# Kernel tuning notes

Hardware: AMD Instinct MI355X
Metric: run time of the kernel (lower is better)

## Reference

```python
import jax, jax.numpy as jnp
import numpy as np

NS, NG, NV = 16, 8, 8          # scalar, gate, vector(l=1) multiplicities
CIN = 8                        # input irreps: 8x0
COUT1 = NS + NG + 3 * NV       # 48 channels into gate
CMID = NS + 3 * NV             # 40 channels after gate
KS = 3                         # kernel size
NB = 4                         # radial basis count
P = KS ** 3
BN_EPS = 1e-5

EPS3 = (jnp.zeros((3, 3, 3))
        .at[0, 1, 2].set(1.).at[1, 2, 0].set(1.).at[2, 0, 1].set(1.)
        .at[0, 2, 1].set(-1.).at[2, 1, 0].set(-1.).at[1, 0, 2].set(-1.))


def _lattice():
    c = jnp.linspace(-1., 1., KS)
    g = jnp.stack(jnp.meshgrid(c, c, c, indexing='ij'), -1).reshape(-1, 3)  # [P,3]
    r = jnp.linalg.norm(g, axis=-1)
    rhat = jnp.where(r[:, None] > 0., g / jnp.maximum(r, 1e-9)[:, None], 0.)
    sh0 = jnp.ones_like(r)             # Y_0, component normalization
    sh1 = jnp.sqrt(3.) * rhat          # Y_1, component normalization
    # soft_one_hot_linspace(r, 0, 1, NB, 'smooth_finite', cutoff=False)
    centers = jnp.linspace(0., 1., NB)
    step = centers[1] - centers[0]
    d = (r[:, None] - centers[None, :]) / step
    emb = jnp.where(jnp.abs(d) < 1.,
                    1.14136 * jnp.exp(2.) * jnp.exp(-1. / jnp.maximum(1. - d ** 2, 1e-9)),
                    0.)
    return sh0, sh1, emb


def _kernel1(w1, emb, sh0, sh1):
    # per-lattice-point tensor-product weights: 8x0 (x) (0+1) -> 16x0 + 8x0 + 8x1
    W = (emb @ w1) / KS ** 1.5                 # [P, 256]
    w_ss = W[:, :128].reshape(P, CIN, NS)
    w_sg = W[:, 128:192].reshape(P, CIN, NG)
    w_sv = W[:, 192:256].reshape(P, CIN, NV)
    a = 1. / jnp.sqrt(8.)                      # fan-in per output irrep
    Km = jnp.zeros((P, CIN, COUT1))
    Km = Km.at[:, :, :NS].set(a * w_ss * sh0[:, None, None])
    Km = Km.at[:, :, NS:NS + NG].set(a * w_sg * sh0[:, None, None])
    kv = a * jnp.einsum('pij,pm->pijm', w_sv, sh1)
    return Km.at[:, :, NS + NG:].set(kv.reshape(P, CIN, 3 * NV))


def _kernel2(w2, emb, sh0, sh1):
    # (16x0 + 8x1) (x) (0+1) -> 16x0 + 8x0 + 8x1 with l<=1 CG paths
    W = (emb @ w2) / KS ** 1.5                 # [P, 832]
    w_ss = W[:, 0:256].reshape(P, NS, NS)
    w_sg = W[:, 256:384].reshape(P, NS, NG)
    w_sv = W[:, 384:512].reshape(P, NS, NV)
    w_vv0 = W[:, 512:576].reshape(P, NV, NV)
    w_vs = W[:, 576:704].reshape(P, NV, NS)
    w_vg = W[:, 704:768].reshape(P, NV, NG)
    w_vv1 = W[:, 768:832].reshape(P, NV, NV)
    a_s = 1. / jnp.sqrt(16. + 8.)
    a_v = 1. / jnp.sqrt(16. + 8. + 8.)
    Km = jnp.zeros((P, CMID, COUT1))
    Km = Km.at[:, :NS, :NS].set(a_s * w_ss * sh0[:, None, None])
    Km = Km.at[:, :NS, NS:NS + NG].set(a_s * w_sg * sh0[:, None, None])
    Km = Km.at[:, :NS, NS + NG:].set(
        (a_v * jnp.einsum('pij,pm->pijm', w_sv, sh1)).reshape(P, NS, 3 * NV))
    ks = (a_s / jnp.sqrt(3.)) * jnp.einsum('puj,pm->pumj', w_vs, sh1)
    kg = (a_s / jnp.sqrt(3.)) * jnp.einsum('puj,pm->pumj', w_vg, sh1)
    kv0 = a_v * jnp.einsum('puj,p,mn->pumjn', w_vv0, sh0, jnp.eye(3))
    kv1 = (a_v / jnp.sqrt(6.)) * jnp.einsum('puj,msn,ps->pumjn', w_vv1, EPS3, sh1)
    Km = Km.at[:, NS:, :NS].set(ks.reshape(P, 3 * NV, NS))
    Km = Km.at[:, NS:, NS:NS + NG].set(kg.reshape(P, 3 * NV, NG))
    return Km.at[:, NS:, NS + NG:].set((kv0 + kv1).reshape(P, 3 * NV, 3 * NV))


def _conv3d(x, Km, cin):
    ker = Km.reshape(KS, KS, KS, cin, COUT1).transpose(4, 3, 0, 1, 2)  # [O,I,k,k,k]
    return jax.lax.conv_general_dilated(
        x, ker, (1, 1, 1), 'SAME',
        dimension_numbers=('NCDHW', 'OIDHW', 'NCDHW'))


def _batchnorm(x, ws, bs, wv):
    # e3nn BatchNorm, training statistics, reduce='mean'; x channel-last [...,48]
    s = x[..., :NS + NG]
    mu = s.mean(axis=(0, 1, 2, 3))
    s = s - mu
    var = (s ** 2).mean(axis=(0, 1, 2, 3))
    s = s / jnp.sqrt(var + BN_EPS) * ws + bs
    v = x[..., NS + NG:].reshape(x.shape[:-1] + (NV, 3))
    n2 = (v ** 2).sum(-1).mean(axis=(0, 1, 2, 3))   # [NV]
    v = v * (((n2 + BN_EPS) ** -0.5) * wv)[:, None]
    return jnp.concatenate([s, v.reshape(x.shape[:-1] + (3 * NV,))], -1)


def _gate(x):
    # Gate: relu on scalars, sigmoid gates multiply l=1 fields
    s = jax.nn.relu(x[..., :NS])
    g = jax.nn.sigmoid(x[..., NS:NS + NG])
    v = x[..., NS + NG:].reshape(x.shape[:-1] + (NV, 3)) * g[..., None]
    return jnp.concatenate([s, v.reshape(x.shape[:-1] + (3 * NV,))], -1)


def _forward(x, w1, sc1, w2, sc2_s, sc2_v,
             bn1_ws, bn1_bs, bn1_wv, bn2_ws, bn2_bs, bn2_wv):
    sh0, sh1, emb = _lattice()
    y = _conv3d(x, _kernel1(w1, emb, sh0, sh1), CIN)
    y = y.at[:, :NS + NG].add(
        jnp.einsum('bixyz,io->boxyz', x, sc1) / jnp.sqrt(8.))  # self-connection
    y = jnp.moveaxis(y, 1, -1)
    y = _gate(_batchnorm(y, bn1_ws, bn1_bs, bn1_wv))           # dropout p=0: identity
    y = jnp.moveaxis(y, -1, 1)                                 # [B, 40, X, Y, Z]
    z = _conv3d(y, _kernel2(w2, emb, sh0, sh1), CMID)
    z = z.at[:, :NS + NG].add(
        jnp.einsum('bixyz,io->boxyz', y[:, :NS], sc2_s) / jnp.sqrt(16.))
    yv = y[:, NS:].reshape(y.shape[0], NV, 3, *y.shape[2:])
    scv = jnp.einsum('bumxyz,uj->bjmxyz', yv, sc2_v) / jnp.sqrt(8.)
    z = z.at[:, NS + NG:].add(scv.reshape(z.shape[0], 3 * NV, *z.shape[2:]))
    z = jnp.moveaxis(z, 1, -1)
    z = _gate(_batchnorm(z, bn2_ws, bn2_bs, bn2_wv))
    return jnp.moveaxis(z, -1, 1)                              # [B, 40, X, Y, Z]


def setup_inputs() -> dict:
    key = jax.random.key(0)
    ks = jax.random.split(key, 8)
    B, S = 1, 64
    return {
        'x': jax.random.normal(ks[0], (B, CIN, S, S, S), jnp.float32),
        'w1': jax.random.normal(ks[1], (NB, 256), jnp.float32),
        'sc1': jax.random.normal(ks[2], (CIN, NS + NG), jnp.float32),
        'w2': jax.random.normal(ks[3], (NB, 832), jnp.float32),
        'sc2_s': jax.random.normal(ks[4], (NS, NS + NG), jnp.float32),
        'sc2_v': jax.random.normal(ks[5], (NV, NV), jnp.float32),
        'bn1_ws': jnp.ones((NS + NG,), jnp.float32),
        'bn1_bs': jnp.zeros((NS + NG,), jnp.float32),
        'bn1_wv': jnp.ones((NV,), jnp.float32),
        'bn2_ws': jnp.ones((NS + NG,), jnp.float32),
        'bn2_bs': jnp.zeros((NS + NG,), jnp.float32),
        'bn2_wv': jnp.ones((NV,), jnp.float32),
    }


def reference(x, w1, sc1, w2, sc2_s, sc2_v,
              bn1_ws, bn1_bs, bn1_wv, bn2_ws, bn2_bs, bn2_wv):
    return _forward(x, w1, sc1, w2, sc2_s, sc2_v,
                    bn1_ws, bn1_bs, bn1_wv, bn2_ws, bn2_bs, bn2_wv)
```

## Files before the change

kernel.cpp:

```cpp
#include <hip/hip_runtime.h>
#include <math.h>

#define N3 262144


#define TBL_TOTAL 1728

__device__ inline void lattice_emb(int p, float* embr) {
    int i = p / 9, j = (p / 3) % 3, k = p % 3;
    float gx = (float)(i - 1), gy = (float)(j - 1), gz = (float)(k - 1);
    float r = sqrtf(gx * gx + gy * gy + gz * gz);
    const float centers[4] = {0.f, 0.33333334f, 0.6666667f, 1.f};
    const float step = 0.33333334f;
    #pragma unroll
    for (int b = 0; b < 4; b++) {
        float dd = (r - centers[b]) / step;
        float e = 0.f;
        if (fabsf(dd) < 1.f)
            e = 1.14136f * expf(2.f) * expf(-1.f / fmaxf(1.f - dd * dd, 1e-9f));
        embr[b] = e;
    }
}

__global__ __launch_bounds__(256) void build_tables_kernel(
        const float* __restrict__ w1,  const float* __restrict__ sc1,
        const float* __restrict__ w2,  const float* __restrict__ sc2s,
        const float* __restrict__ sc2v, float* __restrict__ T) {
    int gid = blockIdx.x * 256 + threadIdx.x;
    if (gid >= TBL_TOTAL) return;

    const float inv_ks15 = 0.19245008972987526f;
    const float s3   = 1.7320508075688772f;
    const float a1   = 0.35355339059327373f;
    const float a_s  = 0.2041241452319315f;
    const float a_v  = 0.17677669529663687f;
    const float a_s3 = 0.11785113019775793f;
    const float a_v6 = 0.07216878364870322f;

    float embC[4], embF[4];
    lattice_emb(13, embC);
    lattice_emb(22, embF);

    auto WC1 = [&](int c) { float s=0.f;
        #pragma unroll
        for (int b=0;b<4;b++) s += embC[b]*w1[b*256+c]; return s*inv_ks15; };
    auto WF1 = [&](int c) { float s=0.f;
        #pragma unroll
        for (int b=0;b<4;b++) s += embF[b]*w1[b*256+c]; return s*inv_ks15; };
    auto WC2 = [&](int c) { float s=0.f;
        #pragma unroll
        for (int b=0;b<4;b++) s += embC[b]*w2[b*832+c]; return s*inv_ks15; };
    auto WF2 = [&](int c) { float s=0.f;
        #pragma unroll
        for (int b=0;b<4;b++) s += embF[b]*w2[b*832+c]; return s*inv_ks15; };

    float val = 0.f;
    if (gid < 192) {
        int i = gid / 24, o = gid % 24;
        int c = (o < 16) ? i * 16 + o : 128 + i * 8 + (o - 16);
        val = a1 * WC1(c) + a1 * sc1[i * 24 + o];
    } else if (gid < 384) {
        int r = gid - 192; int i = r / 24, o = r % 24;
        int c = (o < 16) ? i * 16 + o : 128 + i * 8 + (o - 16);
        val = a1 * WF1(c);
    } else if (gid < 448) {
        int r = gid - 384; int i = r / 8, jj = r % 8;
        val = a1 * s3 * WF1(192 + i * 8 + jj);
    } else if (gid < 832) {
        int r = gid - 448; int i = r / 24, o = r % 24;
        int c = (o < 16) ? i * 16 + o : 256 + i * 8 + (o - 16);
        val = a_s * WC2(c) + 0.25f * sc2s[i * 24 + o];
    } else if (gid < 1216) {
        int r = gid - 832; int i = r / 24, o = r % 24;
        int c = (o < 16) ? i * 16 + o : 256 + i * 8 + (o - 16);
        val = a_s * WF2(c);
    } else if (gid < 1344) {
        int r = gid - 1216; int i = r / 8, jj = r % 8;
        val = a_v * s3 * WF2(384 + i * 8 + jj);
    } else if (gid < 1536) {
        int r = gid - 1344; int u = r / 24, o = r % 24;
        int c = (o < 16) ? 576 + u * 16 + o : 704 + u * 8 + (o - 16);
        val = a_s3 * s3 * WF2(c);
    } else if (gid < 1600) {
        int r = gid - 1536; int u = r / 8, jj = r % 8;
        val = a_v * WC2(512 + u * 8 + jj) + a1 * sc2v[u * 8 + jj];
    } else if (gid < 1664) {
        int r = gid - 1600; int u = r / 8, jj = r % 8;
        val = a_v * WF2(512 + u * 8 + jj);
    } else {
        int r = gid - 1664; int u = r / 8, jj = r % 8;
        val = a_v6 * s3 * WF2(768 + u * 8 + jj);
    }
    T[gid] = val;
}

__device__ inline float4 f4z() { return make_float4(0.f, 0.f, 0.f, 0.f); }
__device__ inline float4 f4add(float4 a, float4 b) {
    return make_float4(a.x+b.x, a.y+b.y, a.z+b.z, a.w+b.w); }
__device__ inline float4 f4sub(float4 a, float4 b) {
    return make_float4(a.x-b.x, a.y-b.y, a.z-b.z, a.w-b.w); }
__device__ inline float4 f4fma(float s, float4 a, float4 c) {
    return make_float4(fmaf(s,a.x,c.x), fmaf(s,a.y,c.y), fmaf(s,a.z,c.z), fmaf(s,a.w,c.w)); }
__device__ inline float f4sum(float4 a) { return a.x+a.y+a.z+a.w; }
__device__ inline float f4dot(float4 a) { return a.x*a.x+a.y*a.y+a.z*a.z+a.w*a.w; }

#define LQ5(BP, C_, DM_, DP_, HM_, HP_)                                       \
    {                                                                         \
        const float* _p = (BP);                                               \
        C_  = *(const float4*)_p;                                             \
        DM_ = dmok ? *(const float4*)(_p - 4096) : f4z();                     \
        DP_ = dpok ? *(const float4*)(_p + 4096) : f4z();                     \
        HM_ = hmok ? *(const float4*)(_p -   64) : f4z();                     \
        HP_ = hpok ? *(const float4*)(_p +   64) : f4z();                     \
    }

#define WQ(C_, WM_, WP_)                                                      \
    {                                                                         \
        float _lw = __shfl_up((C_).w, 1, 64);                                 \
        float _rw = __shfl_down((C_).x, 1, 64);                               \
        WM_ = make_float4(wL ? 0.f : _lw, (C_).x, (C_).y, (C_).z);            \
        WP_ = make_float4((C_).y, (C_).z, (C_).w, wR ? 0.f : _rw);            \
    }

__global__ __launch_bounds__(128) void conv1_kernel(const float* __restrict__ x,
                                                    const float* __restrict__ Tg,
                                                    float* __restrict__ out,
                                                    float* __restrict__ stats) {
    __shared__ float T[448];
    __shared__ float red[2][48];
    for (int t = threadIdx.x; t < 448; t += 128) T[t] = Tg[t];
    __syncthreads();

    const int ohalf = blockIdx.y;
    int idx = blockIdx.x * 512 + threadIdx.x * 4;
    int w0 = idx & 63, h = (idx >> 6) & 63, d = idx >> 12;
    bool dmok = d > 0, dpok = d < 63, hmok = h > 0, hpok = h < 63;
    bool wL = (w0 == 0), wR = (w0 == 60);

    float4 acc[24];
    #pragma unroll
    for (int o = 0; o < 24; o++) acc[o] = f4z();

    if (ohalf == 0) {
        float4 nc, ndm, ndp, nhm, nhp;
        LQ5(x + idx, nc, ndm, ndp, nhm, nhp);
        #pragma unroll 1
        for (int i = 0; i < 8; i++) {
            float4 c = nc, dmq = ndm, dpq = ndp, hmq = nhm, hpq = nhp;
            if (i < 7) LQ5(x + (i + 1) * N3 + idx, nc, ndm, ndp, nhm, nhp);
            float4 wmq, wpq; WQ(c, wmq, wpq);
            float4 S = f4add(f4add(f4add(dmq, dpq), f4add(hmq, hpq)), f4add(wmq, wpq));
            const float* tc = &T[i * 24];
            const float* tf = &T[192 + i * 24];
            #pragma unroll
            for (int o = 0; o < 24; o++)
                acc[o] = f4fma(tc[o], c, f4fma(tf[o], S, acc[o]));
        }
    } else {
        float4 nc, ndm, ndp, nhm, nhp;
        LQ5(x + idx, nc, ndm, ndp, nhm, nhp);
        #pragma unroll 1
        for (int i = 0; i < 8; i++) {
            float4 c = nc, dmq = ndm, dpq = ndp, hmq = nhm, hpq = nhp;
            if (i < 7) LQ5(x + (i + 1) * N3 + idx, nc, ndm, ndp, nhm, nhp);
            float4 wmq, wpq; WQ(c, wmq, wpq);
            float4 Dd = f4sub(dpq, dmq), Dh = f4sub(hpq, hmq), Dw = f4sub(wpq, wmq);
            const float* tv = &T[384 + i * 8];
            #pragma unroll
            for (int jj = 0; jj < 8; jj++) {
                float wv = tv[jj];
                acc[jj * 3 + 0] = f4fma(wv, Dd, acc[jj * 3 + 0]);
                acc[jj * 3 + 1] = f4fma(wv, Dh, acc[jj * 3 + 1]);
                acc[jj * 3 + 2] = f4fma(wv, Dw, acc[jj * 3 + 2]);
            }
        }
    }

    int obase = ohalf * 24;
    #pragma unroll
    for (int o = 0; o < 24; o++)
        *(float4*)(out + (obase + o) * N3 + idx) = acc[o];

    int lane = threadIdx.x & 63, wvx = threadIdx.x >> 6;
    if (ohalf == 0) {
        #pragma unroll
        for (int q = 0; q < 48; q++) {
            float val = (q < 24) ? f4sum(acc[q]) : f4dot(acc[q - 24]);
            #pragma unroll
            for (int mq = 32; mq >= 1; mq >>= 1) val += __shfl_xor(val, mq, 64);
            if (lane == 0) red[wvx][q] = val;
        }
        __syncthreads();
        if (threadIdx.x < 48)
            atomicAdd(&stats[threadIdx.x], red[0][threadIdx.x] + red[1][threadIdx.x]);
    } else {
        #pragma unroll
        for (int q = 0; q < 24; q++) {
            float val = f4dot(acc[q]);
            #pragma unroll
            for (int mq = 32; mq >= 1; mq >>= 1) val += __shfl_xor(val, mq, 64);
            if (lane == 0) red[wvx][q] = val;
        }
        __syncthreads();
        if (threadIdx.x < 24)
            atomicAdd(&stats[48 + threadIdx.x], red[0][threadIdx.x] + red[1][threadIdx.x]);
    }
}

__global__ __launch_bounds__(128) void conv2_kernel(const float* __restrict__ y,
                                                    const float* __restrict__ Tg,
                                                    float* __restrict__ out,
                                                    float* __restrict__ stats) {
    __shared__ float T[1280];
    __shared__ float red[2][48];
    for (int t = threadIdx.x; t < 1280; t += 128) T[t] = Tg[448 + t];
    __syncthreads();

    const int ohalf = blockIdx.y;
    int idx = blockIdx.x * 512 + threadIdx.x * 4;
    int w0 = idx & 63, h = (idx >> 6) & 63, d = idx >> 12;
    bool dmok = d > 0, dpok = d < 63, hmok = h > 0, hpok = h < 63;
    bool wL = (w0 == 0), wR = (w0 == 60);

    float4 acc[24];
    #pragma unroll
    for (int o = 0; o < 24; o++) acc[o] = f4z();

    if (ohalf == 0) {
        float4 nc, ndm, ndp, nhm, nhp;
        LQ5(y + idx, nc, ndm, ndp, nhm, nhp);
        #pragma unroll 1
        for (int i = 0; i < 16; i++) {
            float4 c = nc, dmq = ndm, dpq = ndp, hmq = nhm, hpq = nhp;
            if (i < 15) LQ5(y + (i + 1) * N3 + idx, nc, ndm, ndp, nhm, nhp);
            float4 wmq, wpq; WQ(c, wmq, wpq);
            float4 S = f4add(f4add(f4add(dmq, dpq), f4add(hmq, hpq)), f4add(wmq, wpq));
            const float* tc = &T[i * 24];
            const float* tf = &T[384 + i * 24];
            #pragma unroll
            for (int o = 0; o < 24; o++)
                acc[o] = f4fma(tc[o], c, f4fma(tf[o], S, acc[o]));
        }
        #pragma unroll 1
        for (int u = 0; u < 8; u++) {
            const float* b0 = y + (16 + u * 3 + 0) * N3 + idx;
            const float* b1 = b0 + N3;
            const float* b2 = b1 + N3;
            float4 qdm = dmok ? *(const float4*)(b0 - 4096) : f4z();
            float4 qdp = dpok ? *(const float4*)(b0 + 4096) : f4z();
            float4 qhm = hmok ? *(const float4*)(b1 -   64) : f4z();
            float4 qhp = hpok ? *(const float4*)(b1 +   64) : f4z();
            float4 c2  = *(const float4*)b2;
            float4 wmq, wpq; WQ(c2, wmq, wpq);
            float4 Dsum = f4add(f4add(f4sub(qdp, qdm), f4sub(qhp, qhm)), f4sub(wpq, wmq));
            const float* tvs = &T[896 + u * 24];
            #pragma unroll
            for (int o = 0; o < 24; o++)
                acc[o] = f4fma(tvs[o], Dsum, acc[o]);
        }
    } else {
        float4 nc, ndm, ndp, nhm, nhp;
        LQ5(y + idx, nc, ndm, ndp, nhm, nhp);
        #pragma unroll 1
        for (int i = 0; i < 16; i++) {
            float4 c = nc, dmq = ndm, dpq = ndp, hmq = nhm, hpq = nhp;
            if (i < 15) LQ5(y + (i + 1) * N3 + idx, nc, ndm, ndp, nhm, nhp);
            float4 wmq, wpq; WQ(c, wmq, wpq);
            float4 Dd = f4sub(dpq, dmq), Dh = f4sub(hpq, hmq), Dw = f4sub(wpq, wmq);
            const float* tv = &T[768 + i * 8];
            #pragma unroll
            for (int jj = 0; jj < 8; jj++) {
                float wv = tv[jj];
                acc[jj * 3 + 0] = f4fma(wv, Dd, acc[jj * 3 + 0]);
                acc[jj * 3 + 1] = f4fma(wv, Dh, acc[jj * 3 + 1]);
                acc[jj * 3 + 2] = f4fma(wv, Dw, acc[jj * 3 + 2]);
            }
        }
        #pragma unroll 1
        for (int u = 0; u < 8; u++) {
            const float* t0c = &T[1088 + u * 8];
            const float* t0f = &T[1152 + u * 8];
            const float* tv1 = &T[1216 + u * 8];
            {
                float4 c, dmq, dpq, hmq, hpq;
                LQ5(y + (16 + u * 3 + 0) * N3 + idx, c, dmq, dpq, hmq, hpq);
                float4 wmq, wpq; WQ(c, wmq, wpq);
                float4 S = f4add(f4add(f4add(dmq, dpq), f4add(hmq, hpq)), f4add(wmq, wpq));
                float4 Dh = f4sub(hpq, hmq), Dw = f4sub(wpq, wmq);
                #pragma unroll
                for (int jj = 0; jj < 8; jj++) {
                    float k1 = tv1[jj];
                    acc[jj * 3 + 0] = f4fma(t0c[jj], c, f4fma(t0f[jj], S, acc[jj * 3 + 0]));
                    acc[jj * 3 + 2] = f4fma(k1, Dh, acc[jj * 3 + 2]);
                    acc[jj * 3 + 1] = f4fma(-k1, Dw, acc[jj * 3 + 1]);
                }
            }
            {
                float4 c, dmq, dpq, hmq, hpq;
                LQ5(y + (16 + u * 3 + 1) * N3 + idx, c, dmq, dpq, hmq, hpq);
                float4 wmq, wpq; WQ(c, wmq, wpq);
                float4 S = f4add(f4add(f4add(dmq, dpq), f4add(hmq, hpq)), f4add(wmq, wpq));
                float4 Dd = f4sub(dpq, dmq), Dw = f4sub(wpq, wmq);
                #pragma unroll
                for (int jj = 0; jj < 8; jj++) {
                    float k1 = tv1[jj];
                    acc[jj * 3 + 1] = f4fma(t0c[jj], c, f4fma(t0f[jj], S, acc[jj * 3 + 1]));
                    acc[jj * 3 + 0] = f4fma(k1, Dw, acc[jj * 3 + 0]);
                    acc[jj * 3 + 2] = f4fma(-k1, Dd, acc[jj * 3 + 2]);
                }
            }
            {
                float4 c, dmq, dpq, hmq, hpq;
                LQ5(y + (16 + u * 3 + 2) * N3 + idx, c, dmq, dpq, hmq, hpq);
                float4 wmq, wpq; WQ(c, wmq, wpq);
                float4 S = f4add(f4add(f4add(dmq, dpq), f4add(hmq, hpq)), f4add(wmq, wpq));
                float4 Dd = f4sub(dpq, dmq), Dh = f4sub(hpq, hmq);
                #pragma unroll
                for (int jj = 0; jj < 8; jj++) {
                    float k1 = tv1[jj];
                    acc[jj * 3 + 2] = f4fma(t0c[jj], c, f4fma(t0f[jj], S, acc[jj * 3 + 2]));
                    acc[jj * 3 + 1] = f4fma(k1, Dd, acc[jj * 3 + 1]);
                    acc[jj * 3 + 0] = f4fma(-k1, Dh, acc[jj * 3 + 0]);
                }
            }
        }
    }

    int obase = ohalf * 24;
    #pragma unroll
    for (int o = 0; o < 24; o++)
        *(float4*)(out + (obase + o) * N3 + idx) = acc[o];

    int lane = threadIdx.x & 63, wvx = threadIdx.x >> 6;
    if (ohalf == 0) {
        #pragma unroll
        for (int q = 0; q < 48; q++) {
            float val = (q < 24) ? f4sum(acc[q]) : f4dot(acc[q - 24]);
            #pragma unroll
            for (int mq = 32; mq >= 1; mq >>= 1) val += __shfl_xor(val, mq, 64);
            if (lane == 0) red[wvx][q] = val;
        }
        __syncthreads();
        if (threadIdx.x < 48)
            atomicAdd(&stats[threadIdx.x], red[0][threadIdx.x] + red[1][threadIdx.x]);
    } else {
        #pragma unroll
        for (int q = 0; q < 24; q++) {
            float val = f4dot(acc[q]);
            #pragma unroll
            for (int mq = 32; mq >= 1; mq >>= 1) val += __shfl_xor(val, mq, 64);
            if (lane == 0) red[wvx][q] = val;
        }
        __syncthreads();
        if (threadIdx.x < 24)
            atomicAdd(&stats[48 + threadIdx.x], red[0][threadIdx.x] + red[1][threadIdx.x]);
    }
}

__global__ __launch_bounds__(128) void bn_gate_kernel(const float* __restrict__ zp,
                                                      const float* __restrict__ stats,
                                                      const float* __restrict__ wsc,
                                                      const float* __restrict__ bsc,
                                                      const float* __restrict__ wvc,
                                                      float* __restrict__ out) {
    __shared__ float sb[56];
    if (threadIdx.x < 32) {
        int t = threadIdx.x;
        const float invN = 1.0f / 262144.0f;
        if (t < 24) {
            float mu = stats[t] * invN;
            float var = stats[24 + t] * invN - mu * mu;
            float inv = rsqrtf(var + 1e-5f);
            sb[t] = wsc[t] * inv;
            sb[24 + t] = bsc[t] - mu * wsc[t] * inv;
        } else {
            int u = t - 24;
            float s2 = stats[48 + u * 3] + stats[48 + u * 3 + 1] + stats[48 + u * 3 + 2];
            sb[48 + u] = wvc[u] * rsqrtf(s2 * invN + 1e-5f);
        }
    }
    __syncthreads();

    int idx = (blockIdx.x * 128 + threadIdx.x) * 4;
    float4 g[8];
    #pragma unroll
    for (int u = 0; u < 8; u++) {
        float4 v = *(const float4*)(zp + (16 + u) * N3 + idx);
        float sc = sb[16 + u], bi = sb[40 + u];
        g[u].x = 1.0f / (1.0f + expf(-(v.x * sc + bi)));
        g[u].y = 1.0f / (1.0f + expf(-(v.y * sc + bi)));
        g[u].z = 1.0f / (1.0f + expf(-(v.z * sc + bi)));
        g[u].w = 1.0f / (1.0f + expf(-(v.w * sc + bi)));
    }
    #pragma unroll
    for (int c = 0; c < 16; c++) {
        float4 v = *(const float4*)(zp + c * N3 + idx);
        float sc = sb[c], bi = sb[24 + c];
        float4 r;
        r.x = fmaxf(v.x * sc + bi, 0.f);
        r.y = fmaxf(v.y * sc + bi, 0.f);
        r.z = fmaxf(v.z * sc + bi, 0.f);
        r.w = fmaxf(v.w * sc + bi, 0.f);
        *(float4*)(out + c * N3 + idx) = r;
    }
    #pragma unroll
    for (int u = 0; u < 8; u++) {
        float sv = sb[48 + u];
        #pragma unroll
        for (int m = 0; m < 3; m++) {
            float4 v = *(const float4*)(zp + (24 + u * 3 + m) * N3 + idx);
            float4 r;
            r.x = v.x * sv * g[u].x;
            r.y = v.y * sv * g[u].y;
            r.z = v.z * sv * g[u].z;
            r.w = v.w * sv * g[u].w;
            *(float4*)(out + (16 + u * 3 + m) * N3 + idx) = r;
        }
    }
}

extern "C" void kernel_launch(void* const* d_in, const int* in_sizes, int n_in,
                              void* d_out, int out_size, void* d_ws, size_t ws_size,
                              hipStream_t stream) {
    const float* x      = (const float*)d_in[0];
    const float* w1     = (const float*)d_in[1];
    const float* sc1    = (const float*)d_in[2];
    const float* w2     = (const float*)d_in[3];
    const float* sc2s   = (const float*)d_in[4];
    const float* sc2v   = (const float*)d_in[5];
    const float* bn1_ws = (const float*)d_in[6];
    const float* bn1_bs = (const float*)d_in[7];
    const float* bn1_wv = (const float*)d_in[8];
    const float* bn2_ws = (const float*)d_in[9];
    const float* bn2_bs = (const float*)d_in[10];
    const float* bn2_wv = (const float*)d_in[11];
    float* out = (float*)d_out;
    char* ws = (char*)d_ws;

    float* Tg     = (float*)(ws + 0);
    float* stats1 = (float*)(ws + 8192);
    float* stats2 = (float*)(ws + 8192 + 512);
    float* bufA   = (float*)(ws + 262144);

    hipMemsetAsync(ws + 8192, 0, 1024, stream);
    hipLaunchKernelGGL(build_tables_kernel, dim3(7), dim3(256), 0, stream,
                       w1, sc1, w2, sc2s, sc2v, Tg);
    hipLaunchKernelGGL(conv1_kernel, dim3(512, 2), dim3(128), 0, stream, x, Tg, bufA, stats1);
    hipLaunchKernelGGL(bn_gate_kernel, dim3(512), dim3(128), 0, stream,
                       bufA, stats1, bn1_ws, bn1_bs, bn1_wv, out);
    hipLaunchKernelGGL(conv2_kernel, dim3(512, 2), dim3(128), 0, stream, out, Tg, bufA, stats2);
    hipLaunchKernelGGL(bn_gate_kernel, dim3(512), dim3(128), 0, stream,
                       bufA, stats2, bn2_ws, bn2_bs, bn2_wv, out);
}
```

Measured before the change: 121.4 us.

## Deepen load prefetch to two stages in conv kernels and retune bn_gate

```diff
diff --git a/kernel.cpp b/kernel.cpp
--- a/kernel.cpp
+++ b/kernel.cpp
@@ -122,10 +122,10 @@
         WP_ = make_float4((C_).y, (C_).z, (C_).w, wR ? 0.f : _rw);            \
     }
 
-__global__ __launch_bounds__(128) void conv1_kernel(const float* __restrict__ x,
-                                                    const float* __restrict__ Tg,
-                                                    float* __restrict__ out,
-                                                    float* __restrict__ stats) {
+__global__ __launch_bounds__(128, 2) void conv1_kernel(const float* __restrict__ x,
+                                                       const float* __restrict__ Tg,
+                                                       float* __restrict__ out,
+                                                       float* __restrict__ stats) {
     __shared__ float T[448];
     __shared__ float red[2][48];
     for (int t = threadIdx.x; t < 448; t += 128) T[t] = Tg[t];
@@ -141,37 +141,66 @@
     #pragma unroll
     for (int o = 0; o < 24; o++) acc[o] = f4z();
 
+    float4 cA, dmA, dpA, hmA, hpA, cB, dmB, dpB, hmB, hpB;
+    LQ5(x + idx,      cA, dmA, dpA, hmA, hpA);
+    LQ5(x + N3 + idx, cB, dmB, dpB, hmB, hpB);
+
     if (ohalf == 0) {
-        float4 nc, ndm, ndp, nhm, nhp;
-        LQ5(x + idx, nc, ndm, ndp, nhm, nhp);
         #pragma unroll 1
-        for (int i = 0; i < 8; i++) {
-            float4 c = nc, dmq = ndm, dpq = ndp, hmq = nhm, hpq = nhp;
-            if (i < 7) LQ5(x + (i + 1) * N3 + idx, nc, ndm, ndp, nhm, nhp);
-            float4 wmq, wpq; WQ(c, wmq, wpq);
-            float4 S = f4add(f4add(f4add(dmq, dpq), f4add(hmq, hpq)), f4add(wmq, wpq));
-            const float* tc = &T[i * 24];
-            const float* tf = &T[192 + i * 24];
-            #pragma unroll
-            for (int o = 0; o < 24; o++)
-                acc[o] = f4fma(tc[o], c, f4fma(tf[o], S, acc[o]));
+        for (int i = 0; i < 8; i += 2) {
+            float4 c = cA, dmq = dmA, dpq = dpA, hmq = hmA, hpq = hpA;
+            if (i + 2 < 8) LQ5(x + (i + 2) * N3 + idx, cA, dmA, dpA, hmA, hpA);
+            {
+                float4 wmq, wpq; WQ(c, wmq, wpq);
+                float4 S = f4add(f4add(f4add(dmq, dpq), f4add(hmq, hpq)), f4add(wmq, wpq));
+                const float* tc = &T[i * 24];
+                const float* tf = &T[192 + i * 24];
+                #pragma unroll
+                for (int o = 0; o < 24; o++)
+                    acc[o] = f4fma(tc[o], c, f4fma(tf[o], S, acc[o]));
+            }
+            float4 c2 = cB, dm2 = dmB, dp2 = dpB, hm2 = hmB, hp2 = hpB;
+            if (i + 3 < 8) LQ5(x + (i + 3) * N3 + idx, cB, dmB, dpB, hmB, hpB);
+            {
+                float4 wmq, wpq; WQ(c2, wmq, wpq);
+                float4 S = f4add(f4add(f4add(dm2, dp2), f4add(hm2, hp2)), f4add(wmq, wpq));
+                const float* tc = &T[(i + 1) * 24];
+                const float* tf = &T[192 + (i + 1) * 24];
+                #pragma unroll
+                for (int o = 0; o < 24; o++)
+                    acc[o] = f4fma(tc[o], c2, f4fma(tf[o], S, acc[o]));
+            }
         }
     } else {
-        float4 nc, ndm, ndp, nhm, nhp;
-        LQ5(x + idx, nc, ndm, ndp, nhm, nhp);
         #pragma unroll 1
-        for (int i = 0; i < 8; i++) {
-            float4 c = nc, dmq = ndm, dpq = ndp, hmq = nhm, hpq = nhp;
-            if (i < 7) LQ5(x + (i + 1) * N3 + idx, nc, ndm, ndp, nhm, nhp);
-            float4 wmq, wpq; WQ(c, wmq, wpq);
-            float4 Dd = f4sub(dpq, dmq), Dh = f4sub(hpq, hmq), Dw = f4sub(wpq, wmq);
-            const float* tv = &T[384 + i * 8];
-            #pragma unroll
-            for (int jj = 0; jj < 8; jj++) {
-                float wv = tv[jj];
-                acc[jj * 3 + 0] = f4fma(wv, Dd, acc[jj * 3 + 0]);
-                acc[jj * 3 + 1] = f4fma(wv, Dh, acc[jj * 3 + 1]);
-                acc[jj * 3 + 2] = f4fma(wv, Dw, acc[jj * 3 + 2]);
+        for (int i = 0; i < 8; i += 2) {
+            float4 c = cA, dmq = dmA, dpq = dpA, hmq = hmA, hpq = hpA;
+            if (i + 2 < 8) LQ5(x + (i + 2) * N3 + idx, cA, dmA, dpA, hmA, hpA);
+            {
+                float4 wmq, wpq; WQ(c, wmq, wpq);
+                float4 Dd = f4sub(dpq, dmq), Dh = f4sub(hpq, hmq), Dw = f4sub(wpq, wmq);
+                const float* tv = &T[384 + i * 8];
+                #pragma unroll
+                for (int jj = 0; jj < 8; jj++) {
+                    float wv = tv[jj];
+                    acc[jj * 3 + 0] = f4fma(wv, Dd, acc[jj * 3 + 0]);
+                    acc[jj * 3 + 1] = f4fma(wv, Dh, acc[jj * 3 + 1]);
+                    acc[jj * 3 + 2] = f4fma(wv, Dw, acc[jj * 3 + 2]);
+                }
+            }
+            float4 c2 = cB, dm2 = dmB, dp2 = dpB, hm2 = hmB, hp2 = hpB;
+            if (i + 3 < 8) LQ5(x + (i + 3) * N3 + idx, cB, dmB, dpB, hmB, hpB);
+            {
+                float4 wmq, wpq; WQ(c2, wmq, wpq);
+                float4 Dd = f4sub(dp2, dm2), Dh = f4sub(hp2, hm2), Dw = f4sub(wpq, wmq);
+                const float* tv = &T[384 + (i + 1) * 8];
+                #pragma unroll
+                for (int jj = 0; jj < 8; jj++) {
+                    float wv = tv[jj];
+                    acc[jj * 3 + 0] = f4fma(wv, Dd, acc[jj * 3 + 0]);
+                    acc[jj * 3 + 1] = f4fma(wv, Dh, acc[jj * 3 + 1]);
+                    acc[jj * 3 + 2] = f4fma(wv, Dw, acc[jj * 3 + 2]);
+                }
             }
         }
     }
@@ -207,10 +236,10 @@
     }
 }
 
-__global__ __launch_bounds__(128) void conv2_kernel(const float* __restrict__ y,
-                                                    const float* __restrict__ Tg,
-                                                    float* __restrict__ out,
-                                                    float* __restrict__ stats) {
+__global__ __launch_bounds__(128, 2) void conv2_kernel(const float* __restrict__ y,
+                                                       const float* __restrict__ Tg,
+                                                       float* __restrict__ out,
+                                                       float* __restrict__ stats) {
     __shared__ float T[1280];
     __shared__ float red[2][48];
     for (int t = threadIdx.x; t < 1280; t += 128) T[t] = Tg[448 + t];
@@ -227,98 +256,167 @@
     for (int o = 0; o < 24; o++) acc[o] = f4z();
 
     if (ohalf == 0) {
-        float4 nc, ndm, ndp, nhm, nhp;
-        LQ5(y + idx, nc, ndm, ndp, nhm, nhp);
+        float4 cA, dmA, dpA, hmA, hpA, cB, dmB, dpB, hmB, hpB;
+        LQ5(y + idx,      cA, dmA, dpA, hmA, hpA);
+        LQ5(y + N3 + idx, cB, dmB, dpB, hmB, hpB);
         #pragma unroll 1
-        for (int i = 0; i < 16; i++) {
-            float4 c = nc, dmq = ndm, dpq = ndp, hmq = nhm, hpq = nhp;
-            if (i < 15) LQ5(y + (i + 1) * N3 + idx, nc, ndm, ndp, nhm, nhp);
-            float4 wmq, wpq; WQ(c, wmq, wpq);
-            float4 S = f4add(f4add(f4add(dmq, dpq), f4add(hmq, hpq)), f4add(wmq, wpq));
-            const float* tc = &T[i * 24];
-            const float* tf = &T[384 + i * 24];
-            #pragma unroll
-            for (int o = 0; o < 24; o++)
-                acc[o] = f4fma(tc[o], c, f4fma(tf[o], S, acc[o]));
+        for (int i = 0; i < 16; i += 2) {
+            float4 c = cA, dmq = dmA, dpq = dpA, hmq = hmA, hpq = hpA;
+            if (i + 2 < 16) LQ5(y + (i + 2) * N3 + idx, cA, dmA, dpA, hmA, hpA);
+            {
+                float4 wmq, wpq; WQ(c, wmq, wpq);
+                float4 S = f4add(f4add(f4add(dmq, dpq), f4add(hmq, hpq)), f4add(wmq, wpq));
+                const float* tc = &T[i * 24];
+                const float* tf = &T[384 + i * 24];
+                #pragma unroll
+                for (int o = 0; o < 24; o++)
+                    acc[o] = f4fma(tc[o], c, f4fma(tf[o], S, acc[o]));
+            }
+            float4 c2 = cB, dm2 = dmB, dp2 = dpB, hm2 = hmB, hp2 = hpB;
+            if (i + 3 < 16) LQ5(y + (i + 3) * N3 + idx, cB, dmB, dpB, hmB, hpB);
+            {
+                float4 wmq, wpq; WQ(c2, wmq, wpq);
+                float4 S = f4add(f4add(f4add(dm2, dp2), f4add(hm2, hp2)), f4add(wmq, wpq));
+                const float* tc = &T[(i + 1) * 24];
+                const float* tf = &T[384 + (i + 1) * 24];
+                #pragma unroll
+                for (int o = 0; o < 24; o++)
+                    acc[o] = f4fma(tc[o], c2, f4fma(tf[o], S, acc[o]));
+            }
+        }
+        float4 admq, adpq, ahmq, ahpq, ac2, bdmq, bdpq, bhmq, bhpq, bc2;
+        {
+            const float* b0 = y + 16 * N3 + idx;
+            admq = dmok ? *(const float4*)(b0 - 4096) : f4z();
+            adpq = dpok ? *(const float4*)(b0 + 4096) : f4z();
+            ahmq = hmok ? *(const float4*)(b0 + N3 - 64) : f4z();
+            ahpq = hpok ? *(const float4*)(b0 + N3 + 64) : f4z();
+            ac2  = *(const float4*)(b0 + 2 * N3);
+        }
+        {
+            const float* b0 = y + 19 * N3 + idx;
+            bdmq = dmok ? *(const float4*)(b0 - 4096) : f4z();
+            bdpq = dpok ? *(const float4*)(b0 + 4096) : f4z();
+            bhmq = hmok ? *(const float4*)(b0 + N3 - 64) : f4z();
+            bhpq = hpok ? *(const float4*)(b0 + N3 + 64) : f4z();
+            bc2  = *(const float4*)(b0 + 2 * N3);
         }
         #pragma unroll 1
-        for (int u = 0; u < 8; u++) {
-            const float* b0 = y + (16 + u * 3 + 0) * N3 + idx;
-            const float* b1 = b0 + N3;
-            const float* b2 = b1 + N3;
-            float4 qdm = dmok ? *(const float4*)(b0 - 4096) : f4z();
-            float4 qdp = dpok ? *(const float4*)(b0 + 4096) : f4z();
-            float4 qhm = hmok ? *(const float4*)(b1 -   64) : f4z();
-            float4 qhp = hpok ? *(const float4*)(b1 +   64) : f4z();
-            float4 c2  = *(const float4*)b2;
-            float4 wmq, wpq; WQ(c2, wmq, wpq);
-            float4 Dsum = f4add(f4add(f4sub(qdp, qdm), f4sub(qhp, qhm)), f4sub(wpq, wmq));
-            const float* tvs = &T[896 + u * 24];
-            #pragma unroll
-            for (int o = 0; o < 24; o++)
-                acc[o] = f4fma(tvs[o], Dsum, acc[o]);
+        for (int u = 0; u < 8; u += 2) {
+            float4 qdm = admq, qdp = adpq, qhm = ahmq, qhp = ahpq, qc2 = ac2;
+            if (u + 2 < 8) {
+                const float* b0 = y + (16 + (u + 2) * 3) * N3 + idx;
+                admq = dmok ? *(const float4*)(b0 - 4096) : f4z();
+                adpq = dpok ? *(const float4*)(b0 + 4096) : f4z();
+                ahmq = hmok ? *(const float4*)(b0 + N3 - 64) : f4z();
+                ahpq = hpok ? *(const float4*)(b0 + N3 + 64) : f4z();
+                ac2  = *(const float4*)(b0 + 2 * N3);
+            }
+            {
+                float4 wmq, wpq; WQ(qc2, wmq, wpq);
+                float4 Dsum = f4add(f4add(f4sub(qdp, qdm), f4sub(qhp, qhm)), f4sub(wpq, wmq));
+                const float* tvs = &T[896 + u * 24];
+                #pragma unroll
+                for (int o = 0; o < 24; o++)
+                    acc[o] = f4fma(tvs[o], Dsum, acc[o]);
+            }
+            float4 rdm = bdmq, rdp = bdpq, rhm = bhmq, rhp = bhpq, rc2 = bc2;
+            if (u + 3 < 8) {
+                const float* b0 = y + (16 + (u + 3) * 3) * N3 + idx;
+                bdmq = dmok ? *(const float4*)(b0 - 4096) : f4z();
+                bdpq = dpok ? *(const float4*)(b0 + 4096) : f4z();
+                bhmq = hmok ? *(const float4*)(b0 + N3 - 64) : f4z();
+                bhpq = hpok ? *(const float4*)(b0 + N3 + 64) : f4z();
+                bc2  = *(const float4*)(b0 + 2 * N3);
+            }
+            {
+                float4 wmq, wpq; WQ(rc2, wmq, wpq);
+                float4 Dsum = f4add(f4add(f4sub(rdp, rdm), f4sub(rhp, rhm)), f4sub(wpq, wmq));
+                const float* tvs = &T[896 + (u + 1) * 24];
+                #pragma unroll
+                for (int o = 0; o < 24; o++)
+                    acc[o] = f4fma(tvs[o], Dsum, acc[o]);
+            }
         }
     } else {
-        float4 nc, ndm, ndp, nhm, nhp;
-        LQ5(y + idx, nc, ndm, ndp, nhm, nhp);
+        float4 cA, dmA, dpA, hmA, hpA, cB, dmB, dpB, hmB, hpB;
+        LQ5(y + idx,      cA, dmA, dpA, hmA, hpA);
+        LQ5(y + N3 + idx, cB, dmB, dpB, hmB, hpB);
         #pragma unroll 1
-        for (int i = 0; i < 16; i++) {
-            float4 c = nc, dmq = ndm, dpq = ndp, hmq = nhm, hpq = nhp;
-            if (i < 15) LQ5(y + (i + 1) * N3 + idx, nc, ndm, ndp, nhm, nhp);
-            float4 wmq, wpq; WQ(c, wmq, wpq);
-            float4 Dd = f4sub(dpq, dmq), Dh = f4sub(hpq, hmq), Dw = f4sub(wpq, wmq);
-            const float* tv = &T[768 + i * 8];
-            #pragma unroll
-            for (int jj = 0; jj < 8; jj++) {
-                float wv = tv[jj];
-                acc[jj * 3 + 0] = f4fma(wv, Dd, acc[jj * 3 + 0]);
-                acc[jj * 3 + 1] = f4fma(wv, Dh, acc[jj * 3 + 1]);
-                acc[jj * 3 + 2] = f4fma(wv, Dw, acc[jj * 3 + 2]);
-            }
-        }
+        for (int i = 0; i < 16; i += 2) {
+            float4 c = cA, dmq = dmA, dpq = dpA, hmq = hmA, hpq = hpA;
+            if (i + 2 < 16) LQ5(y + (i + 2) * N3 + idx, cA, dmA, dpA, hmA, hpA);
+            {
+                float4 wmq, wpq; WQ(c, wmq, wpq);
+                float4 Dd = f4sub(dpq, dmq), Dh = f4sub(hpq, hmq), Dw = f4sub(wpq, wmq);
+                const float* tv = &T[768 + i * 8];
+                #pragma unroll
+                for (int jj = 0; jj < 8; jj++) {
+                    float wv = tv[jj];
+                    acc[jj * 3 + 0] = f4fma(wv, Dd, acc[jj * 3 + 0]);
+                    acc[jj * 3 + 1] = f4fma(wv, Dh, acc[jj * 3 + 1]);
+                    acc[jj * 3 + 2] = f4fma(wv, Dw, acc[jj * 3 + 2]);
+                }
+            }
+            float4 c2 = cB, dm2 = dmB, dp2 = dpB, hm2 = hmB, hp2 = hpB;
+            if (i + 3 < 16) LQ5(y + (i + 3) * N3 + idx, cB, dmB, dpB, hmB, hpB);
+            {
+                float4 wmq, wpq; WQ(c2, wmq, wpq);
+                float4 Dd = f4sub(dp2, dm2), Dh = f4sub(hp2, hm2), Dw = f4sub(wpq, wmq);
+                const float* tv = &T[768 + (i + 1) * 8];
+                #pragma unroll
+                for (int jj = 0; jj < 8; jj++) {
+                    float wv = tv[jj];
+                    acc[jj * 3 + 0] = f4fma(wv, Dd, acc[jj * 3 + 0]);
+                    acc[jj * 3 + 1] = f4fma(wv, Dh, acc[jj * 3 + 1]);
+                    acc[jj * 3 + 2] = f4fma(wv, Dw, acc[jj * 3 + 2]);
+                }
+            }
+        }
+        float4 m0c, m0dm, m0dp, m0hm, m0hp;
+        LQ5(y + 16 * N3 + idx, m0c, m0dm, m0dp, m0hm, m0hp);
         #pragma unroll 1
         for (int u = 0; u < 8; u++) {
             const float* t0c = &T[1088 + u * 8];
             const float* t0f = &T[1152 + u * 8];
             const float* tv1 = &T[1216 + u * 8];
-            {
-                float4 c, dmq, dpq, hmq, hpq;
-                LQ5(y + (16 + u * 3 + 0) * N3 + idx, c, dmq, dpq, hmq, hpq);
-                float4 wmq, wpq; WQ(c, wmq, wpq);
-                float4 S = f4add(f4add(f4add(dmq, dpq), f4add(hmq, hpq)), f4add(wmq, wpq));
-                float4 Dh = f4sub(hpq, hmq), Dw = f4sub(wpq, wmq);
+            float4 c0 = m0c, dm0 = m0dm, dp0 = m0dp, hm0 = m0hm, hp0 = m0hp;
+            if (u + 1 < 8) LQ5(y + (16 + (u + 1) * 3) * N3 + idx, m0c, m0dm, m0dp, m0hm, m0hp);
+            float4 c1, dm1, dp1, hm1, hp1, c2q, dm2, dp2, hm2, hp2;
+            LQ5(y + (16 + u * 3 + 1) * N3 + idx, c1, dm1, dp1, hm1, hp1);
+            LQ5(y + (16 + u * 3 + 2) * N3 + idx, c2q, dm2, dp2, hm2, hp2);
+            {
+                float4 wmq, wpq; WQ(c0, wmq, wpq);
+                float4 S = f4add(f4add(f4add(dm0, dp0), f4add(hm0, hp0)), f4add(wmq, wpq));
+                float4 Dh = f4sub(hp0, hm0), Dw = f4sub(wpq, wmq);
                 #pragma unroll
                 for (int jj = 0; jj < 8; jj++) {
                     float k1 = tv1[jj];
-                    acc[jj * 3 + 0] = f4fma(t0c[jj], c, f4fma(t0f[jj], S, acc[jj * 3 + 0]));
+                    acc[jj * 3 + 0] = f4fma(t0c[jj], c0, f4fma(t0f[jj], S, acc[jj * 3 + 0]));
                     acc[jj * 3 + 2] = f4fma(k1, Dh, acc[jj * 3 + 2]);
                     acc[jj * 3 + 1] = f4fma(-k1, Dw, acc[jj * 3 + 1]);
                 }
             }
             {
-                float4 c, dmq, dpq, hmq, hpq;
-                LQ5(y + (16 + u * 3 + 1) * N3 + idx, c, dmq, dpq, hmq, hpq);
-                float4 wmq, wpq; WQ(c, wmq, wpq);
-                float4 S = f4add(f4add(f4add(dmq, dpq), f4add(hmq, hpq)), f4add(wmq, wpq));
-                float4 Dd = f4sub(dpq, dmq), Dw = f4sub(wpq, wmq);
+                float4 wmq, wpq; WQ(c1, wmq, wpq);
+                float4 S = f4add(f4add(f4add(dm1, dp1), f4add(hm1, hp1)), f4add(wmq, wpq));
+                float4 Dd = f4sub(dp1, dm1), Dw = f4sub(wpq, wmq);
                 #pragma unroll
                 for (int jj = 0; jj < 8; jj++) {
                     float k1 = tv1[jj];
-                    acc[jj * 3 + 1] = f4fma(t0c[jj], c, f4fma(t0f[jj], S, acc[jj * 3 + 1]));
+                    acc[jj * 3 + 1] = f4fma(t0c[jj], c1, f4fma(t0f[jj], S, acc[jj * 3 + 1]));
                     acc[jj * 3 + 0] = f4fma(k1, Dw, acc[jj * 3 + 0]);
                     acc[jj * 3 + 2] = f4fma(-k1, Dd, acc[jj * 3 + 2]);
                 }
             }
             {
-                float4 c, dmq, dpq, hmq, hpq;
-                LQ5(y + (16 + u * 3 + 2) * N3 + idx, c, dmq, dpq, hmq, hpq);
-                float4 wmq, wpq; WQ(c, wmq, wpq);
-                float4 S = f4add(f4add(f4add(dmq, dpq), f4add(hmq, hpq)), f4add(wmq, wpq));
-                float4 Dd = f4sub(dpq, dmq), Dh = f4sub(hpq, hmq);
+                float4 wmq, wpq; WQ(c2q, wmq, wpq);
+                float4 S = f4add(f4add(f4add(dm2, dp2), f4add(hm2, hp2)), f4add(wmq, wpq));
+                float4 Dd = f4sub(dp2, dm2), Dh = f4sub(hp2, hm2);
                 #pragma unroll
                 for (int jj = 0; jj < 8; jj++) {
                     float k1 = tv1[jj];
-                    acc[jj * 3 + 2] = f4fma(t0c[jj], c, f4fma(t0f[jj], S, acc[jj * 3 + 2]));
+                    acc[jj * 3 + 2] = f4fma(t0c[jj], c2q, f4fma(t0f[jj], S, acc[jj * 3 + 2]));
                     acc[jj * 3 + 1] = f4fma(k1, Dd, acc[jj * 3 + 1]);
                     acc[jj * 3 + 0] = f4fma(-k1, Dh, acc[jj * 3 + 0]);
                 }
@@ -357,7 +455,7 @@
     }
 }
 
-__global__ __launch_bounds__(128) void bn_gate_kernel(const float* __restrict__ zp,
+__global__ __launch_bounds__(256) void bn_gate_kernel(const float* __restrict__ zp,
                                                       const float* __restrict__ stats,
                                                       const float* __restrict__ wsc,
                                                       const float* __restrict__ bsc,
@@ -381,40 +479,34 @@
     }
     __syncthreads();
 
-    int idx = (blockIdx.x * 128 + threadIdx.x) * 4;
-    float4 g[8];
+    int idx = (blockIdx.x * 256 + threadIdx.x) * 2;
+    float2 g[8];
     #pragma unroll
     for (int u = 0; u < 8; u++) {
-        float4 v = *(const float4*)(zp + (16 + u) * N3 + idx);
+        float2 v = *(const float2*)(zp + (16 + u) * N3 + idx);
         float sc = sb[16 + u], bi = sb[40 + u];
         g[u].x = 1.0f / (1.0f + expf(-(v.x * sc + bi)));
         g[u].y = 1.0f / (1.0f + expf(-(v.y * sc + bi)));
-        g[u].z = 1.0f / (1.0f + expf(-(v.z * sc + bi)));
-        g[u].w = 1.0f / (1.0f + expf(-(v.w * sc + bi)));
     }
     #pragma unroll
     for (int c = 0; c < 16; c++) {
-        float4 v = *(const float4*)(zp + c * N3 + idx);
+        float2 v = *(const float2*)(zp + c * N3 + idx);
         float sc = sb[c], bi = sb[24 + c];
-        float4 r;
+        float2 r;
         r.x = fmaxf(v.x * sc + bi, 0.f);
         r.y = fmaxf(v.y * sc + bi, 0.f);
-        r.z = fmaxf(v.z * sc + bi, 0.f);
-        r.w = fmaxf(v.w * sc + bi, 0.f);
-        *(float4*)(out + c * N3 + idx) = r;
+        *(float2*)(out + c * N3 + idx) = r;
     }
     #pragma unroll
     for (int u = 0; u < 8; u++) {
         float sv = sb[48 + u];
         #pragma unroll
         for (int m = 0; m < 3; m++) {
-            float4 v = *(const float4*)(zp + (24 + u * 3 + m) * N3 + idx);
-            float4 r;
+            float2 v = *(const float2*)(zp + (24 + u * 3 + m) * N3 + idx);
+            float2 r;
             r.x = v.x * sv * g[u].x;
             r.y = v.y * sv * g[u].y;
-            r.z = v.z * sv * g[u].z;
-            r.w = v.w * sv * g[u].w;
-            *(float4*)(out + (16 + u * 3 + m) * N3 + idx) = r;
+            *(float2*)(out + (16 + u * 3 + m) * N3 + idx) = r;
         }
     }
 }
@@ -446,9 +538,9 @@
     hipLaunchKernelGGL(build_tables_kernel, dim3(7), dim3(256), 0, stream,
                        w1, sc1, w2, sc2s, sc2v, Tg);
     hipLaunchKernelGGL(conv1_kernel, dim3(512, 2), dim3(128), 0, stream, x, Tg, bufA, stats1);
-    hipLaunchKernelGGL(bn_gate_kernel, dim3(512), dim3(128), 0, stream,
+    hipLaunchKernelGGL(bn_gate_kernel, dim3(512), dim3(256), 0, stream,
                        bufA, stats1, bn1_ws, bn1_bs, bn1_wv, out);
     hipLaunchKernelGGL(conv2_kernel, dim3(512, 2), dim3(128), 0, stream, out, Tg, bufA, stats2);
-    hipLaunchKernelGGL(bn_gate_kernel, dim3(512), dim3(128), 0, stream,
+    hipLaunchKernelGGL(bn_gate_kernel, dim3(512), dim3(256), 0, stream,
                        bufA, stats2, bn2_ws, bn2_bs, bn2_wv, out);
 }
```

New measurement: 121.5 us. No clear change (+0.1%).
